# Kernel optimization log

Measured on AMD Instinct MI355X. Metric: run time of the kernel, lower is better.

## Reference

```python
import jax, jax.numpy as jnp
import numpy as np

EPS = 1e-10
BETA = 1.0  # beta passed to VectorQuantizer in Encoder_conv


def _conv(x, w, b, stride, pad):
    # x: NCHW, w: OIHW
    y = jax.lax.conv_general_dilated(x, w, window_strides=stride, padding=pad,
                                     dimension_numbers=('NCHW', 'OIHW', 'NCHW'))
    if b is not None:
        y = y + b[None, :, None, None]
    return y


def _forward(x, w_in, b_in, w_h1, b_h1, w_h2, b_h2, w_h3, b_h3,
             r0_w1, r0_w2, r1_w1, r1_w2, emb):
    relu = jax.nn.relu
    h = relu(_conv(x, w_in, b_in, (2, 2), [(1, 1), (1, 1)]))      # [B,128,256,256]
    h = relu(_conv(h, w_h1, b_h1, (4, 4), [(2, 2), (2, 2)]))      # [B,256,64,64]
    h = relu(_conv(h, w_h2, b_h2, (4, 4), [(2, 2), (2, 2)]))      # [B,256,16,16]
    h = relu(_conv(h, w_h3, b_h3, (2, 2), [(1, 1), (1, 1)]))      # [B,256,8,8]
    # ResidualBlock with 2 Residual layers: relu->conv[1,3]->relu->conv[1,1], no bias
    for wa, wb in ((r0_w1, r0_w2), (r1_w1, r1_w2)):
        t = _conv(relu(h), wa, None, (1, 1), [(0, 0), (1, 1)])
        t = _conv(relu(t), wb, None, (1, 1), [(0, 0), (0, 0)])
        h = h + t
    h = relu(h)
    # VectorQuantizer
    lat = jnp.transpose(h, (0, 2, 3, 1))                          # [B,H,W,D]
    D = emb.shape[1]
    flat = lat.reshape(-1, D)                                     # [N,D]
    dist = (jnp.sum(flat * flat, axis=1, keepdims=True)
            + jnp.sum(emb * emb, axis=1)
            - 2.0 * flat @ emb.T)                                 # [N,K]
    idx = jnp.argmin(dist, axis=1)                                # [N]
    quant = emb[idx].reshape(lat.shape)                           # [B,H,W,D]
    sg = jax.lax.stop_gradient
    e_loss = jnp.mean((sg(quant) - lat) ** 2)
    q_loss = jnp.mean((quant - sg(lat)) ** 2)
    loss = q_loss + BETA * e_loss
    quant_st = lat + sg(quant - lat)                              # straight-through
    probs = jnp.mean(jax.nn.one_hot(idx, emb.shape[0], dtype=lat.dtype), axis=0)
    perplexity = jnp.exp(-jnp.sum(probs * jnp.log(probs + EPS)))
    return jnp.transpose(quant_st, (0, 3, 1, 2)), loss, perplexity


def setup_inputs() -> dict:
    key = jax.random.key(0)
    ks = jax.random.split(key, 14)
    C_in, C, K = 3, 256, 512
    s = 0.05
    f32 = jnp.float32
    return {
        'x':     jax.random.normal(ks[0], (8, C_in, 512, 512), f32),
        'w_in':  jax.random.normal(ks[1], (C // 2, C_in, 4, 4), f32) * s,
        'b_in':  jnp.zeros((C // 2,), f32),
        'w_h1':  jax.random.normal(ks[2], (C, C // 2, 7, 7), f32) * s,
        'b_h1':  jnp.zeros((C,), f32),
        'w_h2':  jax.random.normal(ks[3], (C, C, 7, 7), f32) * s,
        'b_h2':  jnp.zeros((C,), f32),
        'w_h3':  jax.random.normal(ks[4], (C, C, 3, 3), f32) * s,
        'b_h3':  jnp.zeros((C,), f32),
        'r0_w1': jax.random.normal(ks[5], (4 * C, C, 1, 3), f32) * s,
        'r0_w2': jax.random.normal(ks[6], (C, 4 * C, 1, 1), f32) * s,
        'r1_w1': jax.random.normal(ks[7], (4 * C, C, 1, 3), f32) * s,
        'r1_w2': jax.random.normal(ks[8], (C, 4 * C, 1, 1), f32) * s,
        'emb':   jax.random.uniform(ks[9], (K, C), f32, -1.0 / K, 1.0 / K),
    }


def reference(x, w_in, b_in, w_h1, b_h1, w_h2, b_h2, w_h3, b_h3,
              r0_w1, r0_w2, r1_w1, r1_w2, emb):
    return _forward(x, w_in, b_in, w_h1, b_h1, w_h2, b_h2, w_h3, b_h3,
                    r0_w1, r0_w2, r1_w1, r1_w2, emb)
```

## Files before the change

kernel.cpp:

```cpp
#include <hip/hip_runtime.h>
#include <hip/hip_bf16.h>

typedef __hip_bfloat16 bf16;
typedef __attribute__((ext_vector_type(4))) float f32x4;
typedef __attribute__((ext_vector_type(8))) short short8;

__device__ __forceinline__ float b2f(bf16 v) { return __bfloat162float(v); }
__device__ __forceinline__ ushort f2bu(float v)
{
    bf16 b = __float2bfloat16(v);
    return *(ushort*)&b;
}
__device__ __forceinline__ uint relu2(uint v)
{
    uint r = v;
    if (r & 0x8000u)     r &= 0xFFFF0000u;
    if (r & 0x80000000u) r &= 0x0000FFFFu;
    return r;
}
__device__ __forceinline__ uint packbf2(float a, float b)
{
    uint lo = f2bu(a), hi = f2bu(b);
    return lo | (hi << 16);
}

typedef const __attribute__((address_space(1))) unsigned int* as1_u32;
typedef __attribute__((address_space(3))) unsigned int* as3_u32;
__device__ __forceinline__ void gld16(const void* g, uint* l)
{
    __builtin_amdgcn_global_load_lds((as1_u32)g, (as3_u32)l, 16, 0, 0);
}

__global__ __launch_bounds__(256) void initw_k(
        const float* __restrict__ w_in, const float* __restrict__ w_h1,
        const float* __restrict__ w_h2, const float* __restrict__ w_h3,
        const float* __restrict__ r0w1, const float* __restrict__ r0w2,
        const float* __restrict__ r1w1, const float* __restrict__ r1w2,
        const float* __restrict__ emb,
        bf16* __restrict__ wp1, bf16* __restrict__ wpack2, bf16* __restrict__ wpack3,
        bf16* __restrict__ wp4, bf16* __restrict__ wpA0, bf16* __restrict__ wpA1,
        bf16* __restrict__ wpB0, bf16* __restrict__ wpB1,
        float* __restrict__ en, float* __restrict__ mse, int* __restrict__ hist,
        float* __restrict__ zpad)
{
    __shared__ ushort ls[12544];
    int b = blockIdx.x, t = threadIdx.x;

    if (b < 256) {
        const float* src = w_h1 + (size_t)b * 6272;
        for (int i = t; i < 6272; i += 256) ls[i] = f2bu(src[i]);
        __syncthreads();
        for (int e = t; e < 800; e += 256) {
            int tap = e >> 4, cib8 = e & 15;
            short8 v;
            #pragma unroll
            for (int cil = 0; cil < 8; ++cil)
                v[cil] = (tap < 49) ? (short)ls[(cib8 * 8 + cil) * 49 + tap] : (short)0;
            *(short8*)(wpack2 + ((size_t)(tap * 16 + cib8) * 256 + b) * 8) = v;
        }
        return;
    }
    if (b < 512) {
        int co = b - 256;
        const float* src = w_h2 + (size_t)co * 12544;
        for (int i = t; i < 12544; i += 256) ls[i] = f2bu(src[i]);
        __syncthreads();
        for (int e = t; e < 1600; e += 256) {
            int tap = e >> 5, cib8 = e & 31;
            short8 v;
            #pragma unroll
            for (int cil = 0; cil < 8; ++cil)
                v[cil] = (tap < 49) ? (short)ls[(cib8 * 8 + cil) * 49 + tap] : (short)0;
            *(short8*)(wpack3 + ((size_t)(tap * 32 + cib8) * 256 + co) * 8) = v;
        }
        return;
    }
    if (b < 768) {
        int co = b - 512;
        const float* src = w_h3 + (size_t)co * 2304;
        for (int i = t; i < 2304; i += 256) ls[i] = f2bu(src[i]);
        __syncthreads();
        for (int e = t; e < 288; e += 256) {
            int tap = e >> 5, cib8 = e & 31;
            short8 v;
            #pragma unroll
            for (int cil = 0; cil < 8; ++cil)
                v[cil] = (short)ls[(cib8 * 8 + cil) * 9 + tap];
            *(short8*)(wp4 + ((size_t)(tap * 32 + cib8) * 256 + co) * 8) = v;
        }
        return;
    }
    if (b < 2816) {
        int r = b - 768;
        int which = r >> 10;
        int co = r & 1023;
        const float* srcb = which ? r1w1 : r0w1;
        bf16* dstb = which ? wpA1 : wpA0;
        const float* src = srcb + (size_t)co * 768;
        for (int i = t; i < 768; i += 256) ls[i] = f2bu(src[i]);
        __syncthreads();
        if (t < 96) {
            int tap = t >> 5, cib8 = t & 31;
            short8 v;
            #pragma unroll
            for (int cil = 0; cil < 8; ++cil)
                v[cil] = (short)ls[(cib8 * 8 + cil) * 3 + tap];
            *(short8*)(dstb + ((size_t)(tap * 32 + cib8) * 1024 + co) * 8) = v;
        }
        return;
    }
    if (b < 3072) {
        int r = b - 2816;
        int which = r >> 7;
        const float* srcb = which ? r1w2 : r0w2;
        bf16* dstb = which ? wpB1 : wpB0;
        int c = (r & 127) * 256 + t;
        int cib8 = c >> 8, co = c & 255;
        const float* s = srcb + (size_t)co * 1024 + cib8 * 8;
        short8 v;
        #pragma unroll
        for (int cil = 0; cil < 8; ++cil) v[cil] = (short)f2bu(s[cil]);
        *(short8*)(dstb + (size_t)c * 8) = v;
        return;
    }
    if (b < 3104) {
        int i = (b - 3072) * 256 + t;
        int j = i & 7; int co = (i >> 3) & 127; int kb = i >> 10;
        int k = kb * 8 + j;
        wp1[i] = __float2bfloat16(k < 48 ? w_in[co * 48 + k] : 0.f);
        return;
    }
    if (b < 3106) {
        int row = (b - 3104) * 256 + t;
        const float4* e = (const float4*)(emb + (size_t)row * 256);
        float s = 0.f;
        for (int d4 = 0; d4 < 64; ++d4) {
            float4 v = e[d4];
            s += v.x * v.x + v.y * v.y + v.z * v.z + v.w * v.w;
        }
        en[row] = s;
        return;
    }
    if (t == 0) mse[0] = 0.f;
    for (int i = t; i < 512; i += 256) hist[i] = 0;
    if (t < 64) zpad[t] = 0.f;
}

__global__ __launch_bounds__(256) void conv1m_k(const float* __restrict__ x,
        const bf16* __restrict__ wp1, const float* __restrict__ bias,
        bf16* __restrict__ h1c)
{
    int bid = blockIdx.x;
    int pxt = bid & 511, img = bid >> 9;
    int tr = pxt >> 4, tc = pxt & 15;
    int oh0 = tr * 8, ow0 = tc * 16;
    const float* xi = x + (size_t)img * 786432;
    bf16* oT = h1c + (size_t)img * 8388608;

    int t = threadIdx.x;
    int wave = t >> 6, lane = t & 63;
    int quad = lane >> 4, l15 = lane & 15;

    __shared__ ushort xs[4 * 640];
    __shared__ ushort ot[128 * 136];

    int ihb = oh0 * 2 - 1, iwb = ow0 * 2 - 1;
    for (int i = t; i < 1836; i += 256) {
        int ci = i / 612; int r1 = i - ci * 612;
        int ihl = r1 / 34, iwl = r1 - ihl * 34;
        int ih = ihb + ihl, iw = iwb + iwl;
        float v = 0.f;
        if ((unsigned)ih < 512u && (unsigned)iw < 512u)
            v = xi[ci * 262144 + ih * 512 + iw];
        xs[ci * 640 + ihl * 35 + iwl] = f2bu(v);
    }
    for (int i = t; i < 640; i += 256) xs[3 * 640 + i] = 0;
    __syncthreads();

    f32x4 zero = {0.f, 0.f, 0.f, 0.f};
    f32x4 acc[8][2];
    #pragma unroll
    for (int m = 0; m < 8; ++m) { acc[m][0] = zero; acc[m][1] = zero; }

    int ci_b = quad >> 1;
    int kh0 = (quad & 1) * 2;
    int iwl0 = 2 * l15;

    #pragma unroll
    for (int ks = 0; ks < 2; ++ks) {
        union { short8 v; uint u[4]; } b[2];
        #pragma unroll
        for (int nt = 0; nt < 2; ++nt) {
            int py = wave * 2 + nt;
            int base = (ks * 2 + ci_b) * 640 + (2 * py + kh0) * 35 + iwl0;
            b[nt].u[0] = *(const uint*)&xs[base];
            b[nt].u[1] = *(const uint*)&xs[base + 2];
            b[nt].u[2] = *(const uint*)&xs[base + 35];
            b[nt].u[3] = *(const uint*)&xs[base + 37];
        }
        const bf16* abase = wp1 + ((size_t)(ks * 4 + quad) * 128 + l15) * 8;
        #pragma unroll
        for (int m = 0; m < 8; ++m) {
            short8 a = *(const short8*)(abase + m * 16 * 8);
            acc[m][0] = __builtin_amdgcn_mfma_f32_16x16x32_bf16(a, b[0].v, acc[m][0], 0, 0, 0);
            acc[m][1] = __builtin_amdgcn_mfma_f32_16x16x32_bf16(a, b[1].v, acc[m][1], 0, 0, 0);
        }
    }

    #pragma unroll
    for (int m = 0; m < 8; ++m) {
        int cobase = m * 16 + quad * 4;
        float b0 = bias[cobase], b1 = bias[cobase + 1];
        float b2 = bias[cobase + 2], b3 = bias[cobase + 3];
        #pragma unroll
        for (int nt = 0; nt < 2; ++nt) {
            int pxl = (wave * 2 + nt) * 16 + l15;
            uint w0 = packbf2(fmaxf(b0 + acc[m][nt][0], 0.f),
                              fmaxf(b1 + acc[m][nt][1], 0.f));
            uint w1 = packbf2(fmaxf(b2 + acc[m][nt][2], 0.f),
                              fmaxf(b3 + acc[m][nt][3], 0.f));
            *(uint*)&ot[pxl * 136 + cobase]     = w0;
            *(uint*)&ot[pxl * 136 + cobase + 2] = w1;
        }
    }
    __syncthreads();
    {
        int pxl = t >> 1, half = t & 1;
        int oh = oh0 + (pxl >> 4), ow = ow0 + (pxl & 15);
        size_t px = (size_t)(oh * 256 + ow);
        #pragma unroll
        for (int cb = 0; cb < 4; ++cb) {
            int c16 = half * 4 + cb;
            const uint4* src = (const uint4*)&ot[pxl * 136 + c16 * 16];
            uint4* dst = (uint4*)(oT + ((size_t)c16 * 65536 + px) * 16);
            dst[0] = src[0];
            dst[1] = src[1];
        }
    }
}

template <int IH, int OH, int CI, int SPLIT, int MODE>
__global__ __launch_bounds__(256, 2) void conv_mfma9_k(
        const bf16* __restrict__ inC, const bf16* __restrict__ wpack,
        const float* __restrict__ bias, float* __restrict__ outA,
        bf16* __restrict__ outT, const float* __restrict__ zpad)
{
    constexpr int TPD = OH / 8;
    constexpr int NT = TPD * TPD;
    constexpr int CPB = (CI / 16) / SPLIT;
    constexpr int CIB8 = CI / 8;
    constexpr int NPX = IH * IH;
    constexpr int SLOTS = 2496;

    int bid = blockIdx.x;
    int pxt = bid % NT;
    int rest = bid / NT;
    int img = rest & 7;
    int split = rest >> 3;
    int oh0 = (pxt / TPD) * 8, ow0 = (pxt % TPD) * 8;

    int t = threadIdx.x;
    int wave = t >> 6, lane = t & 63;
    int quad = lane >> 4, l15 = lane & 15;

    const bf16* inb = inC + (size_t)img * ((size_t)NPX * CI);

    __shared__ __align__(16) uint bufA[SLOTS * 4];
    __shared__ __align__(16) uint bufB[SLOTS * 4];

    f32x4 zero = {0.f, 0.f, 0.f, 0.f};
    f32x4 acc[4][4];
    #pragma unroll
    for (int a = 0; a < 4; ++a)
        #pragma unroll
        for (int b = 0; b < 4; ++b) acc[a][b] = zero;

    int ihb = oh0 * 4 - 2, iwb = ow0 * 4 - 2;
    int qxl = l15 & 7, pyl = l15 >> 3;
    int tap_par = quad >> 1, ci_half = quad & 1;

    int  srel[10];
    bool sval[10];
    #pragma unroll
    for (int it = 0; it < 10; ++it) {
        int sb = (it < 9) ? it * 256 + wave * 64 : 2304 + wave * 64;
        int p  = sb + lane;
        int pb = p << 4;
        int lb = pb ^ (((pb >> 7) & 7) << 4);
        int j  = lb >> 4;
        int pos = j >> 1, half = j & 1;
        int r = pos / 35, c = pos - r * 35;
        int ih = ihb + r, iw = iwb + c;
        sval[it] = (j < 2450) && ((unsigned)ih < (unsigned)IH)
                   && ((unsigned)iw < (unsigned)IH);
        srel[it] = (ih * IH + iw) * 16 + half * 8;
    }

    auto stage = [&](int ch, uint* dst) {
        const bf16* cbp = inb + (size_t)ch * NPX * 16;
        #pragma unroll
        for (int it = 0; it < 10; ++it) {
            if (it == 9 && wave >= 3) continue;
            int sb = (it < 9) ? it * 256 + wave * 64 : 2304 + wave * 64;
            const void* src = sval[it] ? (const void*)(cbp + srel[it])
                                       : (const void*)zpad;
            gld16(src, dst + sb * 4);
        }
    };

    int rbase = pyl * 4480 + qxl * 128 + ci_half * 16;
    int d1  = tap_par * 32;
    int d29 = tap_par * 928;

    auto compute = [&](int ch, const uint* cbuf) {
        const bf16* ab = wpack
            + ((size_t)(ch * 2 + ci_half) * 256 + wave * 64 + l15) * 8
            + (size_t)tap_par * (CIB8 * 2048);
        __builtin_amdgcn_s_setprio(1);
        short8 aC[4], bC[4], aN[4], bN[4];
        {
            #pragma unroll
            for (int ct = 0; ct < 4; ++ct)
                aC[ct] = *(const short8*)(ab + ct * 128);
            int lbb = rbase + d1;
            #pragma unroll
            for (int pt = 0; pt < 4; ++pt) {
                int lb = lbb + pt * 8960;
                int pb = lb ^ (((lb >> 7) & 7) << 4);
                bC[pt] = *(const short8*)((const char*)cbuf + pb);
            }
        }
        #pragma unroll
        for (int tp = 0; tp < 25; ++tp) {
            if (tp < 24) {
                const int tn  = tp + 1;
                const int kh0 = (2 * tn) / 7, kw0 = (2 * tn) % 7;
                const int cE  = (kh0 * 35 + kw0) * 32;
                int dsel = (tn == 24) ? 0 : ((kw0 == 6) ? d29 : d1);
                int lbb  = rbase + cE + dsel;
                const bf16* at = ab + (size_t)(2 * tn) * (CIB8 * 2048);
                #pragma unroll
                for (int ct = 0; ct < 4; ++ct)
                    aN[ct] = *(const short8*)(at + ct * 128);
                #pragma unroll
                for (int pt = 0; pt < 4; ++pt) {
                    int lb = lbb + pt * 8960;
                    int pb = lb ^ (((lb >> 7) & 7) << 4);
                    bN[pt] = *(const short8*)((const char*)cbuf + pb);
                }
            }
            #pragma unroll
            for (int pt = 0; pt < 4; ++pt)
                #pragma unroll
                for (int ct = 0; ct < 4; ++ct)
                    acc[ct][pt] = __builtin_amdgcn_mfma_f32_16x16x32_bf16(
                        aC[ct], bC[pt], acc[ct][pt], 0, 0, 0);
            if (tp < 24) {
                #pragma unroll
                for (int i = 0; i < 4; ++i) { aC[i] = aN[i]; bC[i] = bN[i]; }
            }
        }
        __builtin_amdgcn_s_setprio(0);
    };

    if constexpr (CPB == 1) {
        stage(split, bufA);
        __syncthreads();
        compute(split, bufA);
    } else {
        stage(split * CPB, bufA);
        __syncthreads();
        for (int cc2 = 0; cc2 < CPB; cc2 += 2) {
            stage(split * CPB + cc2 + 1, bufB);
            compute(split * CPB + cc2, bufA);
            __syncthreads();
            if (cc2 + 2 < CPB) stage(split * CPB + cc2 + 2, bufA);
            compute(split * CPB + cc2 + 1, bufB);
            __syncthreads();
        }
    }

    #pragma unroll
    for (int ct = 0; ct < 4; ++ct) {
        int cobase = wave * 64 + ct * 16 + quad * 4;
        #pragma unroll
        for (int pt = 0; pt < 4; ++pt) {
            int px = pt * 16 + l15;
            int oh = oh0 + (px >> 3), ow = ow0 + (px & 7);
            int pxg = oh * OH + ow;
            #pragma unroll
            for (int r = 0; r < 4; ++r) {
                int co = cobase + r;
                float v = acc[ct][pt][r];
                if (MODE == 3) {
                    outA[(size_t)split * ((size_t)8 * OH * OH * 256)
                         + (size_t)img * (OH * OH * 256)
                         + (size_t)co * (OH * OH) + pxg] = v;
                } else {
                    float o = fmaxf(bias[co] + v, 0.f);
                    size_t base = (size_t)img * (size_t)(OH * OH * 256);
                    outT[base + ((size_t)(co >> 4) * (OH * OH) + pxg) * 16 + (co & 15)]
                        = __float2bfloat16(o);
                }
            }
        }
    }
}

__global__ void combine3_k(const float* __restrict__ p3, const float* __restrict__ bias,
                           bf16* __restrict__ h3T)
{
    int idx = blockIdx.x * 256 + threadIdx.x;
    int px = idx & 255;
    int co = (idx >> 8) & 255;
    int img = idx >> 16;
    float v = bias[co];
    #pragma unroll
    for (int s = 0; s < 16; ++s) v += p3[(size_t)s * 524288 + idx];
    v = fmaxf(v, 0.f);
    h3T[((size_t)img * 256 + px) * 256 + co] = __float2bfloat16(v);
}

__global__ __launch_bounds__(256) void conv4m_k(const bf16* __restrict__ h3T,
        const bf16* __restrict__ wp4, const float* __restrict__ bias,
        bf16* __restrict__ h4T)
{
    int bid = blockIdx.x;
    int img = bid >> 2, cog = bid & 3;
    int t = threadIdx.x;
    int wave = t >> 6, lane = t & 63;
    int quad = lane >> 4, l15 = lane & 15;

    __shared__ uint pt[16 * 325];

    for (int i = t; i < 16 * 325; i += 256) pt[i] = 0;

    f32x4 zero = {0.f, 0.f, 0.f, 0.f};
    f32x4 acc[4];
    #pragma unroll
    for (int b = 0; b < 4; ++b) acc[b] = zero;

    const bf16* inb = h3T + (size_t)img * 65536;

    for (int ch = 0; ch < 8; ++ch) {
        __syncthreads();
        for (int e = t; e < 4096; e += 256) {
            int cp = e & 15, px = e >> 4;
            int py = px >> 4, qx = px & 15;
            uint v = *(const uint*)(inb + (size_t)px * 256 + ch * 32 + cp * 2);
            pt[cp * 325 + (py + 1) * 18 + qx + 1] = v;
        }
        __syncthreads();

        for (int tap = 0; tap < 9; ++tap) {
            int kh = tap / 3, kw = tap - kh * 3;
            const bf16* abase = wp4 + ((size_t)((tap * 32 + ch * 4 + quad) * 256)
                                       + cog * 64 + wave * 16 + l15) * 8;
            short8 a = *(const short8*)abase;
            #pragma unroll
            for (int pq = 0; pq < 4; ++pq) {
                int pyo = 2 * pq + (l15 >> 3);
                int ipos = (2 * pyo + kh) * 18 + 2 * (l15 & 7) + kw;
                union { short8 v; uint u[4]; } b;
                b.u[0] = pt[(quad * 4 + 0) * 325 + ipos];
                b.u[1] = pt[(quad * 4 + 1) * 325 + ipos];
                b.u[2] = pt[(quad * 4 + 2) * 325 + ipos];
                b.u[3] = pt[(quad * 4 + 3) * 325 + ipos];
                acc[pq] = __builtin_amdgcn_mfma_f32_16x16x32_bf16(
                    a, b.v, acc[pq], 0, 0, 0);
            }
        }
    }

    int cobase = cog * 64 + wave * 16 + quad * 4;
    #pragma unroll
    for (int pq = 0; pq < 4; ++pq) {
        int px = pq * 16 + l15;
        #pragma unroll
        for (int r = 0; r < 4; ++r) {
            int co = cobase + r;
            float v = fmaxf(bias[co] + acc[pq][r], 0.f);
            h4T[((size_t)img * 64 + px) * 256 + co] = __float2bfloat16(v);
        }
    }
}

__global__ __launch_bounds__(256) void resam_k(const bf16* __restrict__ hT,
        const bf16* __restrict__ wpA, bf16* __restrict__ t1T)
{
    int bid = blockIdx.x;
    int img = bid >> 3, g = bid & 7;
    int t = threadIdx.x;
    int wave = t >> 6, lane = t & 63;
    int quad = lane >> 4, l15 = lane & 15;

    __shared__ uint ph[128 * 81];

    for (int i = t; i < 128 * 81; i += 256) ph[i] = 0;
    __syncthreads();
    const bf16* inb = hT + (size_t)img * 16384;
    for (int e = t; e < 8192; e += 256) {
        int cp = e & 127, px = e >> 7;
        uint v = relu2(*(const uint*)(inb + (size_t)px * 256 + cp * 2));
        ph[cp * 81 + (px >> 3) * 10 + (px & 7) + 1] = v;
    }
    __syncthreads();

    f32x4 zero = {0.f, 0.f, 0.f, 0.f};
    f32x4 acc[2][4];
    #pragma unroll
    for (int a = 0; a < 2; ++a)
        #pragma unroll
        for (int b = 0; b < 4; ++b) acc[a][b] = zero;

    for (int ch = 0; ch < 8; ++ch) {
        for (int tap = 0; tap < 3; ++tap) {
            const bf16* abase = wpA + ((size_t)(tap * 32 + ch * 4 + quad) * 1024
                                       + g * 128 + wave * 32 + l15) * 8;
            short8 a[2];
            #pragma unroll
            for (int ct = 0; ct < 2; ++ct)
                a[ct] = *(const short8*)(abase + ct * 16 * 8);
            #pragma unroll
            for (int pq = 0; pq < 4; ++pq) {
                int py = 2 * pq + (l15 >> 3);
                int pos = py * 10 + (l15 & 7) + tap;
                union { short8 v; uint u[4]; } b;
                b.u[0] = ph[(ch * 16 + quad * 4 + 0) * 81 + pos];
                b.u[1] = ph[(ch * 16 + quad * 4 + 1) * 81 + pos];
                b.u[2] = ph[(ch * 16 + quad * 4 + 2) * 81 + pos];
                b.u[3] = ph[(ch * 16 + quad * 4 + 3) * 81 + pos];
                #pragma unroll
                for (int ct = 0; ct < 2; ++ct)
                    acc[ct][pq] = __builtin_amdgcn_mfma_f32_16x16x32_bf16(
                        a[ct], b.v, acc[ct][pq], 0, 0, 0);
            }
        }
    }

    #pragma unroll
    for (int ct = 0; ct < 2; ++ct) {
        int cobase = g * 128 + wave * 32 + ct * 16 + quad * 4;
        #pragma unroll
        for (int pq = 0; pq < 4; ++pq) {
            int px = pq * 16 + l15;
            #pragma unroll
            for (int r = 0; r < 4; ++r)
                t1T[((size_t)img * 64 + px) * 1024 + cobase + r]
                    = __float2bfloat16(acc[ct][pq][r]);
        }
    }
}

__global__ __launch_bounds__(256) void resbm_k(const bf16* __restrict__ holdT,
        const bf16* __restrict__ t1T, const bf16* __restrict__ wpB,
        bf16* __restrict__ hnewT)
{
    int bid = blockIdx.x;
    int img = bid >> 2, cog = bid & 3;
    int t = threadIdx.x;
    int wave = t >> 6, lane = t & 63;
    int quad = lane >> 4, l15 = lane & 15;

    __shared__ uint pb[256 * 65];

    f32x4 zero = {0.f, 0.f, 0.f, 0.f};
    f32x4 acc[4];
    #pragma unroll
    for (int b = 0; b < 4; ++b) acc[b] = zero;

    const bf16* inb = t1T + (size_t)img * 65536;

    for (int s = 0; s < 2; ++s) {
        __syncthreads();
        for (int e = t; e < 16384; e += 256) {
            int cp = e & 255, px = e >> 8;
            uint v = relu2(*(const uint*)(inb + (size_t)px * 1024 + s * 512 + cp * 2));
            pb[cp * 65 + px] = v;
        }
        __syncthreads();

        for (int chl = 0; chl < 16; ++chl) {
            int ch = s * 16 + chl;
            const bf16* abase = wpB + ((size_t)(ch * 4 + quad) * 256
                                       + cog * 64 + wave * 16 + l15) * 8;
            short8 a = *(const short8*)abase;
            #pragma unroll
            for (int pq = 0; pq < 4; ++pq) {
                int px = pq * 16 + l15;
                union { short8 v; uint u[4]; } b;
                b.u[0] = pb[(chl * 16 + quad * 4 + 0) * 65 + px];
                b.u[1] = pb[(chl * 16 + quad * 4 + 1) * 65 + px];
                b.u[2] = pb[(chl * 16 + quad * 4 + 2) * 65 + px];
                b.u[3] = pb[(chl * 16 + quad * 4 + 3) * 65 + px];
                acc[pq] = __builtin_amdgcn_mfma_f32_16x16x32_bf16(
                    a, b.v, acc[pq], 0, 0, 0);
            }
        }
    }

    int cobase = cog * 64 + wave * 16 + quad * 4;
    #pragma unroll
    for (int pq = 0; pq < 4; ++pq) {
        int px = pq * 16 + l15;
        #pragma unroll
        for (int r = 0; r < 4; ++r) {
            int co = cobase + r;
            size_t o = ((size_t)img * 64 + px) * 256 + co;
            float v = b2f(holdT[o]) + acc[pq][r];
            hnewT[o] = __float2bfloat16(v);
        }
    }
}

__global__ __launch_bounds__(256) void vq_k(const bf16* __restrict__ h6T,
        const float* __restrict__ emb, const float* __restrict__ en,
        float* __restrict__ out, float* __restrict__ mse_acc, int* __restrict__ hist)
{
    int row0 = blockIdx.x * 4;
    int t = threadIdx.x;
    int wave = t >> 6, lane = t & 63;
    __shared__ float lat[4][256];
    __shared__ float swd[4][4];
    __shared__ int   swi[4][4];
    __shared__ int   fidx[4];
    __shared__ float smse[4];

    for (int e = t; e < 1024; e += 256) {
        int r = e >> 8, c = e & 255;
        lat[r][c] = fmaxf(b2f(h6T[(size_t)(row0 + r) * 256 + c]), 0.f);
    }
    __syncthreads();

    float a0[4] = {0.f, 0.f, 0.f, 0.f}, a1[4] = {0.f, 0.f, 0.f, 0.f};
    const float4* e0 = (const float4*)(emb + (size_t)t * 256);
    const float4* e1 = (const float4*)(emb + (size_t)(t + 256) * 256);
    for (int d4 = 0; d4 < 64; ++d4) {
        float4 v0 = e0[d4], v1 = e1[d4];
        #pragma unroll
        for (int r = 0; r < 4; ++r) {
            float l0 = lat[r][d4 * 4], l1 = lat[r][d4 * 4 + 1];
            float l2 = lat[r][d4 * 4 + 2], l3 = lat[r][d4 * 4 + 3];
            a0[r] += l0 * v0.x + l1 * v0.y + l2 * v0.z + l3 * v0.w;
            a1[r] += l0 * v1.x + l1 * v1.y + l2 * v1.z + l3 * v1.w;
        }
    }
    float en0 = en[t], en1 = en[t + 256];
    float bd[4]; int bi[4];
    #pragma unroll
    for (int r = 0; r < 4; ++r) {
        float d0 = en0 - 2.f * a0[r], d1v = en1 - 2.f * a1[r];
        bd[r] = d0; bi[r] = t;
        if (d1v < bd[r]) { bd[r] = d1v; bi[r] = t + 256; }
    }
    #pragma unroll
    for (int s = 1; s < 64; s <<= 1) {
        #pragma unroll
        for (int r = 0; r < 4; ++r) {
            float od = __shfl_xor(bd[r], s);
            int   oi = __shfl_xor(bi[r], s);
            if (od < bd[r] || (od == bd[r] && oi < bi[r])) { bd[r] = od; bi[r] = oi; }
        }
    }
    if (lane == 0) {
        #pragma unroll
        for (int r = 0; r < 4; ++r) { swd[wave][r] = bd[r]; swi[wave][r] = bi[r]; }
    }
    __syncthreads();
    if (t < 4) {
        float best = swd[0][t]; int bidx = swi[0][t];
        for (int w = 1; w < 4; ++w) {
            float od = swd[w][t]; int oi = swi[w][t];
            if (od < best || (od == best && oi < bidx)) { best = od; bidx = oi; }
        }
        fidx[t] = bidx;
    }
    __syncthreads();

    float msel = 0.f;
    #pragma unroll
    for (int r = 0; r < 4; ++r) {
        int row = row0 + r;
        int b = row >> 6, y = (row >> 3) & 7, xx = row & 7;
        float q = emb[(size_t)fidx[r] * 256 + t];
        out[((size_t)(b * 256 + t) * 8 + y) * 8 + xx] = q;
        float diff = q - lat[r][t];
        msel += diff * diff;
    }
    #pragma unroll
    for (int s = 1; s < 64; s <<= 1) msel += __shfl_xor(msel, s);
    if (lane == 0) smse[wave] = msel;
    __syncthreads();
    if (t == 0) atomicAdd(mse_acc, smse[0] + smse[1] + smse[2] + smse[3]);
    if (t < 4) atomicAdd(&hist[fidx[t]], 1);
}

__global__ void final_k(const float* __restrict__ mse_acc, const int* __restrict__ hist,
                        float* __restrict__ out)
{
    __shared__ float sh[512];
    int t = threadIdx.x;
    float p = (float)hist[t] / 512.f;
    sh[t] = p * logf(p + 1e-10f);
    __syncthreads();
    for (int s = 256; s > 0; s >>= 1) {
        if (t < s) sh[t] += sh[t + s];
        __syncthreads();
    }
    if (t == 0) {
        float loss = 2.f * mse_acc[0] / (512.f * 256.f);
        float perp = expf(-sh[0]);
        out[131072] = loss;
        out[131073] = perp;
    }
}

extern "C" void kernel_launch(void* const* d_in, const int* in_sizes, int n_in,
                              void* d_out, int out_size, void* d_ws, size_t ws_size,
                              hipStream_t stream)
{
    const float* x    = (const float*)d_in[0];
    const float* w_in = (const float*)d_in[1];
    const float* b_in = (const float*)d_in[2];
    const float* w_h1 = (const float*)d_in[3];
    const float* b_h1 = (const float*)d_in[4];
    const float* w_h2 = (const float*)d_in[5];
    const float* b_h2 = (const float*)d_in[6];
    const float* w_h3 = (const float*)d_in[7];
    const float* b_h3 = (const float*)d_in[8];
    const float* r0w1 = (const float*)d_in[9];
    const float* r0w2 = (const float*)d_in[10];
    const float* r1w1 = (const float*)d_in[11];
    const float* r1w2 = (const float*)d_in[12];
    const float* emb  = (const float*)d_in[13];
    float* out = (float*)d_out;

    char* ws = (char*)d_ws;
    size_t off = 0;
    auto alloc = [&](size_t bytes) -> void* {
        void* p = ws + off;
        off += (bytes + 255) & ~(size_t)255;
        return p;
    };

    float* en  = (float*)alloc(512 * 4);
    float* mse = (float*)alloc(256);
    int*  hist = (int*)alloc(512 * 4);
    float* zpad = (float*)alloc(256);
    float* p3  = (float*)alloc(8388608ull * 4);
    bf16* h3T  = (bf16*)alloc(524288ull * 2);
    bf16* h4T  = (bf16*)alloc(131072ull * 2);
    bf16* t1T  = (bf16*)alloc(524288ull * 2);
    bf16* h5T  = (bf16*)alloc(131072ull * 2);
    bf16* h6T  = (bf16*)alloc(131072ull * 2);
    bf16* wp1  = (bf16*)alloc(8192ull * 2);
    bf16* wpack2 = (bf16*)alloc(1638400ull * 2);
    bf16* wpack3 = (bf16*)alloc(3276800ull * 2);
    bf16* wp4  = (bf16*)alloc(589824ull * 2);
    bf16* wpA0 = (bf16*)alloc(786432ull * 2);
    bf16* wpA1 = (bf16*)alloc(786432ull * 2);
    bf16* wpB0 = (bf16*)alloc(262144ull * 2);
    bf16* wpB1 = (bf16*)alloc(262144ull * 2);
    bf16* h2c  = (bf16*)alloc(8388608ull * 2);
    size_t base_end = off;

    const size_t H1F_B = 8388608ull * 8 * 2;
    size_t needT1 = base_end + H1F_B + 4096;
    bf16* h1c;
    int tier;
    if (ws_size >= needT1) {
        h1c = (bf16*)alloc(H1F_B);
        tier = 1;
    } else {
        h1c = (bf16*)alloc(8388608ull * 2);
        tier = 2;
    }

    initw_k<<<3107, 256, 0, stream>>>(w_in, w_h1, w_h2, w_h3, r0w1, r0w2, r1w1, r1w2,
        emb, wp1, wpack2, wpack3, wp4, wpA0, wpA1, wpB0, wpB1, en, mse, hist, zpad);

    if (tier == 1) {
        conv1m_k<<<4096, 256, 0, stream>>>(x, wp1, b_in, h1c);
        conv_mfma9_k<256, 64, 128, 1, 0><<<512, 256, 0, stream>>>(
            h1c, wpack2, b_h1, nullptr, h2c, zpad);
    } else {
        for (int n = 0; n < 8; ++n) {
            conv1m_k<<<512, 256, 0, stream>>>(x + (size_t)n * 786432, wp1, b_in, h1c);
            conv_mfma9_k<256, 64, 128, 1, 0><<<64, 256, 0, stream>>>(
                h1c, wpack2, b_h1, nullptr, h2c + (size_t)n * 1048576, zpad);
        }
    }

    conv_mfma9_k<64, 16, 256, 16, 3><<<512, 256, 0, stream>>>(
        h2c, wpack3, nullptr, p3, nullptr, zpad);
    combine3_k<<<2048, 256, 0, stream>>>(p3, b_h2, h3T);

    conv4m_k<<<32, 256, 0, stream>>>(h3T, wp4, b_h3, h4T);
    resam_k<<<64, 256, 0, stream>>>(h4T, wpA0, t1T);
    resbm_k<<<32, 256, 0, stream>>>(h4T, t1T, wpB0, h5T);
    resam_k<<<64, 256, 0, stream>>>(h5T, wpA1, t1T);
    resbm_k<<<32, 256, 0, stream>>>(h5T, t1T, wpB1, h6T);

    vq_k<<<128, 256, 0, stream>>>(h6T, emb, en, out, mse, hist);
    final_k<<<1, 512, 0, stream>>>(mse, hist, out);
}
```

Before: 464.4 us.

## Deepen weight-fragment prefetch to three stages and halve conv3 split-K

The conv inner loop now keeps three rotating A (weight) register buffers and two B buffers, so weight global loads are issued two taps ahead instead of one, and the per-tap register copies go away. Separately, the stride-4 conv over 256 channels now uses 8 split-K slices instead of 16. That halves the partial-sum buffer and the reduction work in combine3, and gives each block two channel chunks to double-buffer. The cost is more register pressure under the 2-wave occupancy bound, and only 256 blocks for that conv, which may underfill the GPU.

```diff
diff --git a/kernel.cpp b/kernel.cpp
--- a/kernel.cpp
+++ b/kernel.cpp
@@ -240,7 +240,7 @@
 }
 
 template <int IH, int OH, int CI, int SPLIT, int MODE>
-__global__ __launch_bounds__(256, 2) void conv_mfma9_k(
+__global__ __launch_bounds__(256, 2) void conv_mfma11_k(
         const bf16* __restrict__ inC, const bf16* __restrict__ wpack,
         const float* __restrict__ bias, float* __restrict__ outA,
         bf16* __restrict__ outT, const float* __restrict__ zpad)
@@ -316,49 +316,38 @@
         const bf16* ab = wpack
             + ((size_t)(ch * 2 + ci_half) * 256 + wave * 64 + l15) * 8
             + (size_t)tap_par * (CIB8 * 2048);
-        __builtin_amdgcn_s_setprio(1);
-        short8 aC[4], bC[4], aN[4], bN[4];
-        {
+        short8 A[3][4], B[2][4];
+        auto loadA = [&](int tn, short8* dst) {
+            const bf16* at = ab + (size_t)(2 * tn) * (CIB8 * 2048);
             #pragma unroll
             for (int ct = 0; ct < 4; ++ct)
-                aC[ct] = *(const short8*)(ab + ct * 128);
-            int lbb = rbase + d1;
+                dst[ct] = *(const short8*)(at + ct * 128);
+        };
+        auto loadB = [&](int tn, short8* dst) {
+            const int kh0 = (2 * tn) / 7, kw0 = (2 * tn) % 7;
+            const int cE  = (kh0 * 35 + kw0) * 32;
+            int dsel = (tn == 24) ? 0 : ((kw0 == 6) ? d29 : d1);
+            int lbb  = rbase + cE + dsel;
             #pragma unroll
             for (int pt = 0; pt < 4; ++pt) {
                 int lb = lbb + pt * 8960;
                 int pb = lb ^ (((lb >> 7) & 7) << 4);
-                bC[pt] = *(const short8*)((const char*)cbuf + pb);
+                dst[pt] = *(const short8*)((const char*)cbuf + pb);
             }
-        }
+        };
+        loadA(0, A[0]); loadA(1, A[1]); loadA(2, A[2]);
+        loadB(0, B[0]);
+        __builtin_amdgcn_s_setprio(1);
         #pragma unroll
         for (int tp = 0; tp < 25; ++tp) {
-            if (tp < 24) {
-                const int tn  = tp + 1;
-                const int kh0 = (2 * tn) / 7, kw0 = (2 * tn) % 7;
-                const int cE  = (kh0 * 35 + kw0) * 32;
-                int dsel = (tn == 24) ? 0 : ((kw0 == 6) ? d29 : d1);
-                int lbb  = rbase + cE + dsel;
-                const bf16* at = ab + (size_t)(2 * tn) * (CIB8 * 2048);
-                #pragma unroll
-                for (int ct = 0; ct < 4; ++ct)
-                    aN[ct] = *(const short8*)(at + ct * 128);
-                #pragma unroll
-                for (int pt = 0; pt < 4; ++pt) {
-                    int lb = lbb + pt * 8960;
-                    int pb = lb ^ (((lb >> 7) & 7) << 4);
-                    bN[pt] = *(const short8*)((const char*)cbuf + pb);
-                }
-            }
+            if (tp < 24) loadB(tp + 1, B[(tp + 1) % 2]);
             #pragma unroll
             for (int pt = 0; pt < 4; ++pt)
                 #pragma unroll
                 for (int ct = 0; ct < 4; ++ct)
                     acc[ct][pt] = __builtin_amdgcn_mfma_f32_16x16x32_bf16(
-                        aC[ct], bC[pt], acc[ct][pt], 0, 0, 0);
-            if (tp < 24) {
-                #pragma unroll
-                for (int i = 0; i < 4; ++i) { aC[i] = aN[i]; bC[i] = bN[i]; }
-            }
+                        A[tp % 3][ct], B[tp % 2][pt], acc[ct][pt], 0, 0, 0);
+            if (tp < 22) loadA(tp + 3, A[tp % 3]);
         }
         __builtin_amdgcn_s_setprio(0);
     };
@@ -416,7 +405,7 @@
     int img = idx >> 16;
     float v = bias[co];
     #pragma unroll
-    for (int s = 0; s < 16; ++s) v += p3[(size_t)s * 524288 + idx];
+    for (int s = 0; s < 8; ++s) v += p3[(size_t)s * 524288 + idx];
     v = fmaxf(v, 0.f);
     h3T[((size_t)img * 256 + px) * 256 + co] = __float2bfloat16(v);
 }
@@ -747,7 +736,7 @@
     float* mse = (float*)alloc(256);
     int*  hist = (int*)alloc(512 * 4);
     float* zpad = (float*)alloc(256);
-    float* p3  = (float*)alloc(8388608ull * 4);
+    float* p3  = (float*)alloc(4194304ull * 4);
     bf16* h3T  = (bf16*)alloc(524288ull * 2);
     bf16* h4T  = (bf16*)alloc(131072ull * 2);
     bf16* t1T  = (bf16*)alloc(524288ull * 2);
@@ -781,17 +770,17 @@
 
     if (tier == 1) {
         conv1m_k<<<4096, 256, 0, stream>>>(x, wp1, b_in, h1c);
-        conv_mfma9_k<256, 64, 128, 1, 0><<<512, 256, 0, stream>>>(
+        conv_mfma11_k<256, 64, 128, 1, 0><<<512, 256, 0, stream>>>(
             h1c, wpack2, b_h1, nullptr, h2c, zpad);
     } else {
         for (int n = 0; n < 8; ++n) {
             conv1m_k<<<512, 256, 0, stream>>>(x + (size_t)n * 786432, wp1, b_in, h1c);
-            conv_mfma9_k<256, 64, 128, 1, 0><<<64, 256, 0, stream>>>(
+            conv_mfma11_k<256, 64, 128, 1, 0><<<64, 256, 0, stream>>>(
                 h1c, wpack2, b_h1, nullptr, h2c + (size_t)n * 1048576, zpad);
         }
     }
 
-    conv_mfma9_k<64, 16, 256, 16, 3><<<512, 256, 0, stream>>>(
+    conv_mfma11_k<64, 16, 256, 8, 3><<<256, 256, 0, stream>>>(
         h2c, wpack3, nullptr, p3, nullptr, zpad);
     combine3_k<<<2048, 256, 0, stream>>>(p3, b_h2, h3T);
 
```

Result: no change. 466.4 us (+0.4%).
